# Performance work log

Measured on AMD Instinct MI355X. Metric: run time of the kernel, lower is better.

Reference implementation:

```python
import jax, jax.numpy as jnp
import numpy as np

B, N, K, C = 8, 4096, 32, 64
RADIUS = 0.15
CIN = C + 3  # dp_fj: concat(dp[3], fj[C])


def _ball_query(p, radius, k):
    """p: (B,N,3). Returns neighbor indices (B,N,K): first k points (in index
    order) within radius of each query, padded with the first valid neighbor
    (ballquery semantics; query point itself is always index 0 candidate)."""
    sq = jnp.sum(p * p, axis=-1)                                  # (B,N)
    d2 = sq[:, :, None] + sq[:, None, :] - 2.0 * jnp.einsum('bnd,bmd->bnm', p, p)
    n = p.shape[1]
    within = d2 <= radius * radius
    key = jnp.where(within, jnp.arange(n, dtype=jnp.int32)[None, None, :], n)
    order = jnp.argsort(key, axis=-1)[..., :k]                    # (B,N,K)
    valid = jnp.take_along_axis(key, order, axis=-1) < n
    first = order[..., :1]
    return jnp.where(valid, order, first)


def _conv2d_1x1(x, w, b):
    # x: (B,Cin,N,K), w: (Cout,Cin), b: (Cout,)
    return jnp.einsum('oi,bink->bonk', w, x) + b[None, :, None, None]


def _conv1d_1x1(x, w, b):
    # x: (B,Cin,N)
    return jnp.einsum('oi,bin->bon', w, x) + b[None, :, None]


def setup_inputs() -> dict:
    key = jax.random.key(0)
    ks = jax.random.split(key, 16)
    s = 0.05
    inp = {
        'p': jax.random.uniform(ks[0], (B, N, 3), dtype=jnp.float32),
        'f': jax.random.normal(ks[1], (B, C, N), dtype=jnp.float32),
        # attn_local: convblock2d (CIN -> C), no act
        'w_attn': jax.random.normal(ks[2], (C, CIN), dtype=jnp.float32) * s,
        'b_attn': jnp.zeros((C,), jnp.float32),
        # convs: convblock2d (CIN -> C, relu) then (C -> C, no act)
        'w1': jax.random.normal(ks[3], (C, CIN), dtype=jnp.float32) * s,
        'b1': jnp.zeros((C,), jnp.float32),
        'w2': jax.random.normal(ks[4], (C, C), dtype=jnp.float32) * s,
        'b2': jnp.zeros((C,), jnp.float32),
        # ffn: convblock1d (C -> C*expansion=C, relu) then (C -> C, no act)
        'wf1': jax.random.normal(ks[5], (C, C), dtype=jnp.float32) * s,
        'bf1': jnp.zeros((C,), jnp.float32),
        'wf2': jax.random.normal(ks[6], (C, C), dtype=jnp.float32) * s,
        'bf2': jnp.zeros((C,), jnp.float32),
    }
    return inp


def reference(p, f, w_attn, b_attn, w1, b1, w2, b2, wf1, bf1, wf2, bf2):
    bidx = jnp.arange(B)[:, None, None]
    idx = _ball_query(p, RADIUS, K)                               # (B,N,K) int
    pj = p[bidx, idx]                                             # (B,N,K,3)
    dp = (pj - p[:, :, None, :]).transpose(0, 3, 1, 2)            # (B,3,N,K)
    ft = f.transpose(0, 2, 1)                                     # (B,N,C)
    fj = ft[bidx, idx].transpose(0, 3, 1, 2)                      # (B,C,N,K)

    fj_cat = jnp.concatenate([dp, fj], axis=1)                    # (B,CIN,N,K)

    attn = _conv2d_1x1(fj_cat, w_attn, b_attn)                    # (B,C,N,K)
    x = jax.nn.relu(_conv2d_1x1(fj_cat, w1, b1))
    x = _conv2d_1x1(x, w2, b2)                                    # (B,C,N,K)

    # new_attention, 4D path: softmax over neighbor axis (tau=1), weighted sum
    channel_attn = jax.nn.softmax(attn, axis=-1)
    fout = jnp.sum(channel_attn * x, axis=-1)                     # (B,C,N)

    fout = jax.nn.relu(fout + f)
    identity = fout
    h = jax.nn.relu(_conv1d_1x1(fout, wf1, bf1))
    h = _conv1d_1x1(h, wf2, bf2)
    fout = jax.nn.relu(h + identity)                              # use_res
    return (p, fout)
```

## Files before the change

### kernel.cpp

```cpp
#include <hip/hip_runtime.h>

#define B_ 8
#define N_ 4096
#define K_ 32
#define C_ 64
#define CIN_ 67
#define R2_ 0.0225f

#define SFJ 104
#define SY1 72
#define SFB 72
#define PTS 4
#define ITERS 4

typedef short short8v __attribute__((ext_vector_type(8)));
typedef short short4v __attribute__((ext_vector_type(4)));
typedef float floatx4 __attribute__((ext_vector_type(4)));

__device__ __forceinline__ short f2bf(float x) {
    unsigned u = __float_as_uint(x);
    u += 0x7fffu + ((u >> 16) & 1u);
    return (short)(u >> 16);
}

template <int CTRL>
__device__ __forceinline__ float dpp_add(float x) {
    const int m = __builtin_amdgcn_update_dpp(0, __float_as_int(x), CTRL, 0xF, 0xF, false);
    return x + __int_as_float(m);
}
__device__ __forceinline__ float row16_sum(float x) {
    x = dpp_add<0xB1>(x);
    x = dpp_add<0x4E>(x);
    x = dpp_add<0x141>(x);
    x = dpp_add<0x140>(x);
    return x;
}

__global__ __launch_bounds__(256) void prep_kernel(
    const float* __restrict__ p, const float* __restrict__ f,
    unsigned short* __restrict__ ftb, float4* __restrict__ p4,
    float* __restrict__ pout)
{
#pragma clang fp contract(off)
    __shared__ short tile[64 * 72];
    const int t = threadIdx.x;
    const int b = blockIdx.x >> 6;
    const int n0 = (blockIdx.x & 63) * 64;
    const int nn4 = t & 15, ch = t >> 4;
    for (int cc = 0; cc < 4; ++cc) {
        const int c = cc * 16 + ch;
        const float4 v = *(const float4*)&f[((size_t)(b * 64 + c)) * N_ + n0 + nn4 * 4];
        tile[(nn4 * 4 + 0) * 72 + c] = f2bf(v.x);
        tile[(nn4 * 4 + 1) * 72 + c] = f2bf(v.y);
        tile[(nn4 * 4 + 2) * 72 + c] = f2bf(v.z);
        tile[(nn4 * 4 + 3) * 72 + c] = f2bf(v.w);
    }
    if (t < 48) {
        const size_t base = ((size_t)(b * N_ + n0)) * 3;
        ((float4*)(pout + base))[t] = ((const float4*)(p + base))[t];
    }
    if (t < 64) {
        const int n = n0 + t;
        const float x = p[((size_t)(b * N_ + n)) * 3 + 0];
        const float y = p[((size_t)(b * N_ + n)) * 3 + 1];
        const float z = p[((size_t)(b * N_ + n)) * 3 + 2];
        const float sq = (x * x + y * y) + z * z;
        p4[(size_t)b * N_ + n] = make_float4(x, y, z, sq);
    }
    __syncthreads();
    const int nn = t >> 2, cb = (t & 3) * 16;
    uint4* dst = (uint4*)&ftb[((size_t)(b * N_ + n0 + nn)) * 64 + cb];
    const uint4* src = (const uint4*)&tile[nn * 72 + cb];
    dst[0] = src[0];
    dst[1] = src[1];
}

__global__ __launch_bounds__(256) void ball_query_kernel(
    const float4* __restrict__ p4, unsigned short* __restrict__ idx)
{
#pragma clang fp contract(off)
    const int lane = threadIdx.x & 63;
    const int wid = (blockIdx.x * blockDim.x + threadIdx.x) >> 6;
    const int q0 = wid * 4;
    const int b = q0 >> 12;
    const float4* pb = p4 + (size_t)b * N_;

    float4 Q[4];
    #pragma unroll
    for (int q = 0; q < 4; ++q)
        Q[q] = pb[(q0 + q) & (N_ - 1)];
    int count[4] = {0, 0, 0, 0};
    int first[4] = {-1, -1, -1, -1};
    for (int base = 0; base < N_; base += 64) {
        const float4 A = pb[base + lane];
        unsigned long long m[4];
        bool w[4];
        #pragma unroll
        for (int q = 0; q < 4; ++q) {
            const float d2 = (Q[q].w + A.w)
                - 2.0f * ((Q[q].x * A.x + Q[q].y * A.y) + Q[q].z * A.z);
            w[q] = (d2 <= R2_);
            m[q] = __ballot(w[q]);
        }
        const unsigned long long below = (1ull << lane) - 1ull;
        #pragma unroll
        for (int q = 0; q < 4; ++q) {
            if (m[q]) {
                if (first[q] < 0) first[q] = base + __builtin_ctzll(m[q]);
                if (w[q]) {
                    const int pos = count[q] + __popcll(m[q] & below);
                    if (pos < K_)
                        idx[(size_t)(q0 + q) * K_ + pos] = (unsigned short)(base + lane);
                }
                count[q] += __popcll(m[q]);
            }
        }
        if (count[0] >= K_ && count[1] >= K_ && count[2] >= K_ && count[3] >= K_)
            break;
    }
    #pragma unroll
    for (int q = 0; q < 4; ++q)
        for (int pos = count[q] + lane; pos < K_; pos += 64)
            idx[(size_t)(q0 + q) * K_ + pos] = (unsigned short)first[q];
}

__global__ __launch_bounds__(256, 3) void lpa_mfma_kernel(
    const float4* __restrict__ p4, const float* __restrict__ f,
    const unsigned short* __restrict__ ftb,
    const float* __restrict__ w_attn, const float* __restrict__ b_attn,
    const float* __restrict__ w1, const float* __restrict__ b1,
    const float* __restrict__ w2, const float* __restrict__ b2,
    const float* __restrict__ wf1, const float* __restrict__ bf1,
    const float* __restrict__ wf2, const float* __restrict__ bf2,
    const unsigned short* __restrict__ idx, float* __restrict__ out)
{
    __shared__ __align__(16) short s_fj[128 * SFJ];
    __shared__ __align__(16) short s_y1[128 * SY1];
    __shared__ __align__(16) short s_fbuf[2 * 16 * SFB];
    __shared__ float s_vec[PTS * 64];
    short* s_vecbf = s_fbuf;
    short* s_hbf   = s_fbuf + 16 * SFB;

    const int t = threadIdx.x;
    const int lane = t & 63;
    const int mb = t >> 6;
    const int l15 = lane & 15;
    const int quad = lane >> 4;

    short8v wa_f[3], w1_f[3], w2_f[2], wf1_f[2], wf2_f[2];
    {
        const int cm = mb * 16 + l15;
        #pragma unroll
        for (int ks = 0; ks < 3; ++ks) {
            short8v a, bq;
            #pragma unroll
            for (int j = 0; j < 8; ++j) {
                const int ip = ks * 32 + quad * 8 + j;
                float va = 0.0f, vb = 0.0f;
                if (ip < 64)      { va = w_attn[cm * CIN_ + ip + 3];  vb = w1[cm * CIN_ + ip + 3]; }
                else if (ip < 67) { va = w_attn[cm * CIN_ + ip - 64]; vb = w1[cm * CIN_ + ip - 64]; }
                a[j] = f2bf(va); bq[j] = f2bf(vb);
            }
            wa_f[ks] = a; w1_f[ks] = bq;
        }
        #pragma unroll
        for (int ks = 0; ks < 2; ++ks) {
            short8v a, bq, cq;
            #pragma unroll
            for (int j = 0; j < 8; ++j) {
                const int kk = ks * 32 + quad * 8 + j;
                a[j]  = f2bf(w2[cm * 64 + kk]);
                bq[j] = f2bf(wf1[cm * 64 + kk]);
                cq[j] = f2bf(wf2[cm * 64 + kk]);
            }
            w2_f[ks] = a; wf1_f[ks] = bq; wf2_f[ks] = cq;
        }
    }

    const int crow = mb * 16 + quad * 4;
    const float4 bav  = *(const float4*)&b_attn[crow];
    const float4 b1v  = *(const float4*)&b1[crow];
    const float4 b2v  = *(const float4*)&b2[crow];
    const float4 bf1v = *(const float4*)&bf1[crow];
    const float4 bf2v = *(const float4*)&bf2[crow];

    for (int e = t; e < 512; e += 256) {
        const int col = e >> 2, c4 = e & 3;
        *(uint4*)&s_fj[col * SFJ + 72 + c4 * 8] = make_uint4(0u, 0u, 0u, 0u);
    }
    for (int e = t; e < 1152; e += 256) ((unsigned*)s_fbuf)[e] = 0u;

    const int pt00 = blockIdx.x * (PTS * ITERS);
    const int bb = pt00 >> 12;
    const float4* pb = p4 + (size_t)bb * N_;

    for (int itn = 0; itn < ITERS; ++itn) {
        const int pt0 = pt00 + itn * PTS;

        {
            const int col = t >> 1, h = t & 1;
            const int j = idx[(size_t)pt0 * K_ + col];
            const uint4* src = (const uint4*)&ftb[((size_t)(bb * N_ + j)) * 64 + h * 32];
            uint4* dst = (uint4*)&s_fj[col * SFJ + h * 32];
            dst[0] = src[0]; dst[1] = src[1]; dst[2] = src[2]; dst[3] = src[3];
            if (h) {
                const int n = (pt0 + (col >> 5)) & (N_ - 1);
                const float4 Pj = pb[j];
                const float4 Pn = pb[n];
                short8v dp = {};
                dp[0] = f2bf(Pj.x - Pn.x);
                dp[1] = f2bf(Pj.y - Pn.y);
                dp[2] = f2bf(Pj.z - Pn.z);
                *(short8v*)&s_fj[col * SFJ + 64] = dp;
            }
        }
        __syncthreads();

        floatx4 accA[8];
        #pragma unroll
        for (int nt = 0; nt < 8; ++nt) {
            const short* bp = &s_fj[(nt * 16 + l15) * SFJ + quad * 8];
            const short8v fb0 = *(const short8v*)(bp);
            const short8v fb1 = *(const short8v*)(bp + 32);
            const short8v fb2 = *(const short8v*)(bp + 64);
            floatx4 a = {0.f, 0.f, 0.f, 0.f};
            a = __builtin_amdgcn_mfma_f32_16x16x32_bf16(wa_f[0], fb0, a, 0, 0, 0);
            a = __builtin_amdgcn_mfma_f32_16x16x32_bf16(wa_f[1], fb1, a, 0, 0, 0);
            a = __builtin_amdgcn_mfma_f32_16x16x32_bf16(wa_f[2], fb2, a, 0, 0, 0);
            accA[nt] = a;
            floatx4 y = {0.f, 0.f, 0.f, 0.f};
            y = __builtin_amdgcn_mfma_f32_16x16x32_bf16(w1_f[0], fb0, y, 0, 0, 0);
            y = __builtin_amdgcn_mfma_f32_16x16x32_bf16(w1_f[1], fb1, y, 0, 0, 0);
            y = __builtin_amdgcn_mfma_f32_16x16x32_bf16(w1_f[2], fb2, y, 0, 0, 0);
            short4v yp;
            yp[0] = f2bf(fmaxf(y[0] + b1v.x, 0.f));
            yp[1] = f2bf(fmaxf(y[1] + b1v.y, 0.f));
            yp[2] = f2bf(fmaxf(y[2] + b1v.z, 0.f));
            yp[3] = f2bf(fmaxf(y[3] + b1v.w, 0.f));
            *(short4v*)&s_y1[(nt * 16 + l15) * SY1 + crow] = yp;
        }
        __syncthreads();

        floatx4 accX[8];
        #pragma unroll
        for (int nt = 0; nt < 8; ++nt) {
            const short* bp = &s_y1[(nt * 16 + l15) * SY1 + quad * 8];
            const short8v yb0 = *(const short8v*)(bp);
            const short8v yb1 = *(const short8v*)(bp + 32);
            floatx4 x = {0.f, 0.f, 0.f, 0.f};
            x = __builtin_amdgcn_mfma_f32_16x16x32_bf16(w2_f[0], yb0, x, 0, 0, 0);
            x = __builtin_amdgcn_mfma_f32_16x16x32_bf16(w2_f[1], yb1, x, 0, 0, 0);
            accX[nt] = x;
        }

        #pragma unroll
        for (int pi = 0; pi < PTS; ++pi) {
            const int n = (pt0 + pi) & (N_ - 1);
            float fo[4];
            #pragma unroll
            for (int r = 0; r < 4; ++r) {
                const float ba = (r == 0) ? bav.x : (r == 1) ? bav.y : (r == 2) ? bav.z : bav.w;
                const float bx = (r == 0) ? b2v.x : (r == 1) ? b2v.y : (r == 2) ? b2v.z : b2v.w;
                const float e0 = __expf(accA[2 * pi][r] + ba);
                const float e1 = __expf(accA[2 * pi + 1][r] + ba);
                const float se = row16_sum(e0 + e1);
                const float sw = row16_sum(e0 * (accX[2 * pi][r] + bx)
                                         + e1 * (accX[2 * pi + 1][r] + bx));
                const float fres = f[((size_t)(bb * 64 + crow + r)) * N_ + n];
                fo[r] = fmaxf(sw * __builtin_amdgcn_rcpf(se) + fres, 0.f);
            }
            if (l15 == 0) {
                *(float4*)&s_vec[pi * 64 + crow] = make_float4(fo[0], fo[1], fo[2], fo[3]);
                short4v fb;
                fb[0] = f2bf(fo[0]); fb[1] = f2bf(fo[1]);
                fb[2] = f2bf(fo[2]); fb[3] = f2bf(fo[3]);
                *(short4v*)&s_vecbf[pi * SFB + crow] = fb;
            }
        }
        __syncthreads();

        {
            const short8v vb0 = *(const short8v*)&s_vecbf[l15 * SFB + quad * 8];
            const short8v vb1 = *(const short8v*)&s_vecbf[l15 * SFB + 32 + quad * 8];
            floatx4 d = {0.f, 0.f, 0.f, 0.f};
            d = __builtin_amdgcn_mfma_f32_16x16x32_bf16(wf1_f[0], vb0, d, 0, 0, 0);
            d = __builtin_amdgcn_mfma_f32_16x16x32_bf16(wf1_f[1], vb1, d, 0, 0, 0);
            if (l15 < PTS) {
                short4v hb;
                hb[0] = f2bf(fmaxf(d[0] + bf1v.x, 0.f));
                hb[1] = f2bf(fmaxf(d[1] + bf1v.y, 0.f));
                hb[2] = f2bf(fmaxf(d[2] + bf1v.z, 0.f));
                hb[3] = f2bf(fmaxf(d[3] + bf1v.w, 0.f));
                *(short4v*)&s_hbf[l15 * SFB + crow] = hb;
            }
        }
        __syncthreads();

        {
            const short8v hb0 = *(const short8v*)&s_hbf[l15 * SFB + quad * 8];
            const short8v hb1 = *(const short8v*)&s_hbf[l15 * SFB + 32 + quad * 8];
            floatx4 d = {0.f, 0.f, 0.f, 0.f};
            d = __builtin_amdgcn_mfma_f32_16x16x32_bf16(wf2_f[0], hb0, d, 0, 0, 0);
            d = __builtin_amdgcn_mfma_f32_16x16x32_bf16(wf2_f[1], hb1, d, 0, 0, 0);
            if (l15 < PTS) {
                const int n = (pt0 + l15) & (N_ - 1);
                out[((size_t)(bb * 64 + crow + 0)) * N_ + n] =
                    fmaxf(d[0] + bf2v.x + s_vec[l15 * 64 + crow + 0], 0.f);
                out[((size_t)(bb * 64 + crow + 1)) * N_ + n] =
                    fmaxf(d[1] + bf2v.y + s_vec[l15 * 64 + crow + 1], 0.f);
                out[((size_t)(bb * 64 + crow + 2)) * N_ + n] =
                    fmaxf(d[2] + bf2v.z + s_vec[l15 * 64 + crow + 2], 0.f);
                out[((size_t)(bb * 64 + crow + 3)) * N_ + n] =
                    fmaxf(d[3] + bf2v.w + s_vec[l15 * 64 + crow + 3], 0.f);
            }
        }
    }
}

extern "C" void kernel_launch(void* const* d_in, const int* in_sizes, int n_in,
                              void* d_out, int out_size, void* d_ws, size_t ws_size,
                              hipStream_t stream)
{
    const float* p      = (const float*)d_in[0];
    const float* f      = (const float*)d_in[1];
    const float* w_attn = (const float*)d_in[2];
    const float* b_attn = (const float*)d_in[3];
    const float* w1     = (const float*)d_in[4];
    const float* b1     = (const float*)d_in[5];
    const float* w2     = (const float*)d_in[6];
    const float* b2     = (const float*)d_in[7];
    const float* wf1    = (const float*)d_in[8];
    const float* bf1    = (const float*)d_in[9];
    const float* wf2    = (const float*)d_in[10];
    const float* bf2    = (const float*)d_in[11];
    float* out = (float*)d_out;

    unsigned short* idx = (unsigned short*)d_ws;
    unsigned short* ftb = (unsigned short*)((char*)d_ws + 2u * 1024 * 1024);
    float4* p4          = (float4*)((char*)d_ws + 6u * 1024 * 1024);

    prep_kernel<<<B_ * (N_ / 64), 256, 0, stream>>>(p, f, ftb, p4, out);
    ball_query_kernel<<<(B_ * N_) / 16, 256, 0, stream>>>(p4, idx);
    lpa_mfma_kernel<<<(B_ * N_) / (PTS * ITERS), 256, 0, stream>>>(
        p4, f, ftb, w_attn, b_attn, w1, b1, w2, b2, wf1, bf1, wf2, bf2,
        idx, out + (size_t)B_ * N_ * 3);
}
```

Baseline: 229.6 us.

## Replace padded LDS tiles with XOR-swizzled layout and split dp buffer

Drops the padded row strides in shared memory and uses unpadded 64-element rows with an XOR swizzle on 8-element chunks, so MFMA operand loads and stores avoid bank conflicts with less LDS. The three dp channels move to a separate small buffer that only quad 0 feeds into the third K-slice, which removes the zero-padding of the feature tile. Launch bounds rise from 3 to 4 blocks per SM to use the freed LDS for occupancy, at the risk of more register pressure.

```diff
diff --git a/kernel.cpp b/kernel.cpp
--- a/kernel.cpp
+++ b/kernel.cpp
@@ -7,9 +7,6 @@
 #define CIN_ 67
 #define R2_ 0.0225f
 
-#define SFJ 104
-#define SY1 72
-#define SFB 72
 #define PTS 4
 #define ITERS 4
 
@@ -124,7 +121,7 @@
             idx[(size_t)(q0 + q) * K_ + pos] = (unsigned short)first[q];
 }
 
-__global__ __launch_bounds__(256, 3) void lpa_mfma_kernel(
+__global__ __launch_bounds__(256, 4) void lpa_mfma_kernel(
     const float4* __restrict__ p4, const float* __restrict__ f,
     const unsigned short* __restrict__ ftb,
     const float* __restrict__ w_attn, const float* __restrict__ b_attn,
@@ -134,12 +131,13 @@
     const float* __restrict__ wf2, const float* __restrict__ bf2,
     const unsigned short* __restrict__ idx, float* __restrict__ out)
 {
-    __shared__ __align__(16) short s_fj[128 * SFJ];
-    __shared__ __align__(16) short s_y1[128 * SY1];
-    __shared__ __align__(16) short s_fbuf[2 * 16 * SFB];
+    __shared__ __align__(16) short s_fj[128 * 64];
+    __shared__ __align__(16) short s_dp[128 * 8];
+    __shared__ __align__(16) short s_y1[128 * 64];
+    __shared__ __align__(16) short s_fbuf[2 * 16 * 64];
     __shared__ float s_vec[PTS * 64];
     short* s_vecbf = s_fbuf;
-    short* s_hbf   = s_fbuf + 16 * SFB;
+    short* s_hbf   = s_fbuf + 16 * 64;
 
     const int t = threadIdx.x;
     const int lane = t & 63;
@@ -184,11 +182,7 @@
     const float4 bf1v = *(const float4*)&bf1[crow];
     const float4 bf2v = *(const float4*)&bf2[crow];
 
-    for (int e = t; e < 512; e += 256) {
-        const int col = e >> 2, c4 = e & 3;
-        *(uint4*)&s_fj[col * SFJ + 72 + c4 * 8] = make_uint4(0u, 0u, 0u, 0u);
-    }
-    for (int e = t; e < 1152; e += 256) ((unsigned*)s_fbuf)[e] = 0u;
+    for (int e = t; e < 1024; e += 256) ((unsigned*)s_fbuf)[e] = 0u;
 
     const int pt00 = blockIdx.x * (PTS * ITERS);
     const int bb = pt00 >> 12;
@@ -201,8 +195,12 @@
             const int col = t >> 1, h = t & 1;
             const int j = idx[(size_t)pt0 * K_ + col];
             const uint4* src = (const uint4*)&ftb[((size_t)(bb * N_ + j)) * 64 + h * 32];
-            uint4* dst = (uint4*)&s_fj[col * SFJ + h * 32];
-            dst[0] = src[0]; dst[1] = src[1]; dst[2] = src[2]; dst[3] = src[3];
+            const int rb = col * 64;
+            const int sw = (col & 7) << 3;
+            *(uint4*)&s_fj[rb + ((h * 32 + 0)  ^ sw)] = src[0];
+            *(uint4*)&s_fj[rb + ((h * 32 + 8)  ^ sw)] = src[1];
+            *(uint4*)&s_fj[rb + ((h * 32 + 16) ^ sw)] = src[2];
+            *(uint4*)&s_fj[rb + ((h * 32 + 24) ^ sw)] = src[3];
             if (h) {
                 const int n = (pt0 + (col >> 5)) & (N_ - 1);
                 const float4 Pj = pb[j];
@@ -211,7 +209,7 @@
                 dp[0] = f2bf(Pj.x - Pn.x);
                 dp[1] = f2bf(Pj.y - Pn.y);
                 dp[2] = f2bf(Pj.z - Pn.z);
-                *(short8v*)&s_fj[col * SFJ + 64] = dp;
+                *(short8v*)&s_dp[col * 8] = dp;
             }
         }
         __syncthreads();
@@ -219,10 +217,14 @@
         floatx4 accA[8];
         #pragma unroll
         for (int nt = 0; nt < 8; ++nt) {
-            const short* bp = &s_fj[(nt * 16 + l15) * SFJ + quad * 8];
-            const short8v fb0 = *(const short8v*)(bp);
-            const short8v fb1 = *(const short8v*)(bp + 32);
-            const short8v fb2 = *(const short8v*)(bp + 64);
+            const int row = nt * 16 + l15;
+            const int sw = (l15 & 7) << 3;
+            const short* bp = &s_fj[row * 64];
+            const short8v fb0 = *(const short8v*)(bp + ((quad * 8) ^ sw));
+            const short8v fb1 = *(const short8v*)(bp + ((32 + quad * 8) ^ sw));
+            const short8v dpv = *(const short8v*)&s_dp[row * 8];
+            short8v fb2 = {};
+            if (quad == 0) fb2 = dpv;
             floatx4 a = {0.f, 0.f, 0.f, 0.f};
             a = __builtin_amdgcn_mfma_f32_16x16x32_bf16(wa_f[0], fb0, a, 0, 0, 0);
             a = __builtin_amdgcn_mfma_f32_16x16x32_bf16(wa_f[1], fb1, a, 0, 0, 0);
@@ -237,16 +239,18 @@
             yp[1] = f2bf(fmaxf(y[1] + b1v.y, 0.f));
             yp[2] = f2bf(fmaxf(y[2] + b1v.z, 0.f));
             yp[3] = f2bf(fmaxf(y[3] + b1v.w, 0.f));
-            *(short4v*)&s_y1[(nt * 16 + l15) * SY1 + crow] = yp;
+            *(short4v*)&s_y1[row * 64 + (crow ^ sw)] = yp;
         }
         __syncthreads();
 
         floatx4 accX[8];
         #pragma unroll
         for (int nt = 0; nt < 8; ++nt) {
-            const short* bp = &s_y1[(nt * 16 + l15) * SY1 + quad * 8];
-            const short8v yb0 = *(const short8v*)(bp);
-            const short8v yb1 = *(const short8v*)(bp + 32);
+            const int row = nt * 16 + l15;
+            const int sw = (l15 & 7) << 3;
+            const short* bp = &s_y1[row * 64];
+            const short8v yb0 = *(const short8v*)(bp + ((quad * 8) ^ sw));
+            const short8v yb1 = *(const short8v*)(bp + ((32 + quad * 8) ^ sw));
             floatx4 x = {0.f, 0.f, 0.f, 0.f};
             x = __builtin_amdgcn_mfma_f32_16x16x32_bf16(w2_f[0], yb0, x, 0, 0, 0);
             x = __builtin_amdgcn_mfma_f32_16x16x32_bf16(w2_f[1], yb1, x, 0, 0, 0);
@@ -264,24 +268,25 @@
                 const float e0 = __expf(accA[2 * pi][r] + ba);
                 const float e1 = __expf(accA[2 * pi + 1][r] + ba);
                 const float se = row16_sum(e0 + e1);
-                const float sw = row16_sum(e0 * (accX[2 * pi][r] + bx)
-                                         + e1 * (accX[2 * pi + 1][r] + bx));
+                const float sw_ = row16_sum(e0 * (accX[2 * pi][r] + bx)
+                                          + e1 * (accX[2 * pi + 1][r] + bx));
                 const float fres = f[((size_t)(bb * 64 + crow + r)) * N_ + n];
-                fo[r] = fmaxf(sw * __builtin_amdgcn_rcpf(se) + fres, 0.f);
+                fo[r] = fmaxf(sw_ * __builtin_amdgcn_rcpf(se) + fres, 0.f);
             }
             if (l15 == 0) {
                 *(float4*)&s_vec[pi * 64 + crow] = make_float4(fo[0], fo[1], fo[2], fo[3]);
                 short4v fb;
                 fb[0] = f2bf(fo[0]); fb[1] = f2bf(fo[1]);
                 fb[2] = f2bf(fo[2]); fb[3] = f2bf(fo[3]);
-                *(short4v*)&s_vecbf[pi * SFB + crow] = fb;
+                *(short4v*)&s_vecbf[pi * 64 + (crow ^ ((pi & 7) << 3))] = fb;
             }
         }
         __syncthreads();
 
         {
-            const short8v vb0 = *(const short8v*)&s_vecbf[l15 * SFB + quad * 8];
-            const short8v vb1 = *(const short8v*)&s_vecbf[l15 * SFB + 32 + quad * 8];
+            const int sw = (l15 & 7) << 3;
+            const short8v vb0 = *(const short8v*)&s_vecbf[l15 * 64 + ((quad * 8) ^ sw)];
+            const short8v vb1 = *(const short8v*)&s_vecbf[l15 * 64 + ((32 + quad * 8) ^ sw)];
             floatx4 d = {0.f, 0.f, 0.f, 0.f};
             d = __builtin_amdgcn_mfma_f32_16x16x32_bf16(wf1_f[0], vb0, d, 0, 0, 0);
             d = __builtin_amdgcn_mfma_f32_16x16x32_bf16(wf1_f[1], vb1, d, 0, 0, 0);
@@ -291,14 +296,15 @@
                 hb[1] = f2bf(fmaxf(d[1] + bf1v.y, 0.f));
                 hb[2] = f2bf(fmaxf(d[2] + bf1v.z, 0.f));
                 hb[3] = f2bf(fmaxf(d[3] + bf1v.w, 0.f));
-                *(short4v*)&s_hbf[l15 * SFB + crow] = hb;
+                *(short4v*)&s_hbf[l15 * 64 + (crow ^ sw)] = hb;
             }
         }
         __syncthreads();
 
         {
-            const short8v hb0 = *(const short8v*)&s_hbf[l15 * SFB + quad * 8];
-            const short8v hb1 = *(const short8v*)&s_hbf[l15 * SFB + 32 + quad * 8];
+            const int sw = (l15 & 7) << 3;
+            const short8v hb0 = *(const short8v*)&s_hbf[l15 * 64 + ((quad * 8) ^ sw)];
+            const short8v hb1 = *(const short8v*)&s_hbf[l15 * 64 + ((32 + quad * 8) ^ sw)];
             floatx4 d = {0.f, 0.f, 0.f, 0.f};
             d = __builtin_amdgcn_mfma_f32_16x16x32_bf16(wf2_f[0], hb0, d, 0, 0, 0);
             d = __builtin_amdgcn_mfma_f32_16x16x32_bf16(wf2_f[1], hb1, d, 0, 0, 0);
```

New measurement: 387.0 us. +68.5%, slower.

## Prefetch next iteration's neighbor gather into registers and interleave second conv with softmax

Applied to the files above, without the earlier changes.

Hoists the first neighbor-feature gather out of the loop and, inside each iteration, issues global loads for the next iteration's gathered features and positions into registers before the MFMA work, writing them to shared memory after the first conv. This hides gather latency and removes one barrier per iteration. The second conv is now computed per point inside the softmax loop, which cuts live accumulator registers. The residual f values are loaded as float4 vectors. It also drops the occupancy hint of 3 blocks in the launch bounds, so prefetch registers may raise register pressure and lower occupancy.

```diff
diff --git a/kernel.cpp b/kernel.cpp
--- a/kernel.cpp
+++ b/kernel.cpp
@@ -124,7 +124,7 @@
             idx[(size_t)(q0 + q) * K_ + pos] = (unsigned short)first[q];
 }
 
-__global__ __launch_bounds__(256, 3) void lpa_mfma_kernel(
+__global__ __launch_bounds__(256) void lpa_mfma_kernel(
     const float4* __restrict__ p4, const float* __restrict__ f,
     const unsigned short* __restrict__ ftb,
     const float* __restrict__ w_attn, const float* __restrict__ b_attn,
@@ -194,27 +194,39 @@
     const int bb = pt00 >> 12;
     const float4* pb = p4 + (size_t)bb * N_;
 
+    const int col = t >> 1, h = t & 1;
+
+    {
+        const int j = idx[(size_t)pt00 * K_ + col];
+        const uint4* src = (const uint4*)&ftb[((size_t)(bb * N_ + j)) * 64 + h * 32];
+        uint4* dst = (uint4*)&s_fj[col * SFJ + h * 32];
+        dst[0] = src[0]; dst[1] = src[1]; dst[2] = src[2]; dst[3] = src[3];
+        if (h) {
+            const int n = (pt00 + (col >> 5)) & (N_ - 1);
+            const float4 Pj = pb[j];
+            const float4 Pn = pb[n];
+            short8v dp = {};
+            dp[0] = f2bf(Pj.x - Pn.x);
+            dp[1] = f2bf(Pj.y - Pn.y);
+            dp[2] = f2bf(Pj.z - Pn.z);
+            *(short8v*)&s_fj[col * SFJ + 64] = dp;
+        }
+    }
+    __syncthreads();
+
     for (int itn = 0; itn < ITERS; ++itn) {
         const int pt0 = pt00 + itn * PTS;
 
-        {
-            const int col = t >> 1, h = t & 1;
-            const int j = idx[(size_t)pt0 * K_ + col];
-            const uint4* src = (const uint4*)&ftb[((size_t)(bb * N_ + j)) * 64 + h * 32];
-            uint4* dst = (uint4*)&s_fj[col * SFJ + h * 32];
-            dst[0] = src[0]; dst[1] = src[1]; dst[2] = src[2]; dst[3] = src[3];
-            if (h) {
-                const int n = (pt0 + (col >> 5)) & (N_ - 1);
-                const float4 Pj = pb[j];
-                const float4 Pn = pb[n];
-                short8v dp = {};
-                dp[0] = f2bf(Pj.x - Pn.x);
-                dp[1] = f2bf(Pj.y - Pn.y);
-                dp[2] = f2bf(Pj.z - Pn.z);
-                *(short8v*)&s_fj[col * SFJ + 64] = dp;
-            }
-        }
-        __syncthreads();
+        const bool pf = (itn + 1 < ITERS);
+        uint4 g0, g1, g2, g3;
+        float4 Pjn, Pnn;
+        if (pf) {
+            const int jn = idx[(size_t)(pt0 + PTS) * K_ + col];
+            const uint4* src = (const uint4*)&ftb[((size_t)(bb * N_ + jn)) * 64 + h * 32];
+            g0 = src[0]; g1 = src[1]; g2 = src[2]; g3 = src[3];
+            Pjn = pb[jn];
+            Pnn = pb[(pt0 + PTS + (col >> 5)) & (N_ - 1)];
+        }
 
         floatx4 accA[8];
         #pragma unroll
@@ -241,21 +253,45 @@
         }
         __syncthreads();
 
-        floatx4 accX[8];
-        #pragma unroll
-        for (int nt = 0; nt < 8; ++nt) {
-            const short* bp = &s_y1[(nt * 16 + l15) * SY1 + quad * 8];
-            const short8v yb0 = *(const short8v*)(bp);
-            const short8v yb1 = *(const short8v*)(bp + 32);
-            floatx4 x = {0.f, 0.f, 0.f, 0.f};
-            x = __builtin_amdgcn_mfma_f32_16x16x32_bf16(w2_f[0], yb0, x, 0, 0, 0);
-            x = __builtin_amdgcn_mfma_f32_16x16x32_bf16(w2_f[1], yb1, x, 0, 0, 0);
-            accX[nt] = x;
-        }
+        if (pf) {
+            uint4* dst = (uint4*)&s_fj[col * SFJ + h * 32];
+            dst[0] = g0; dst[1] = g1; dst[2] = g2; dst[3] = g3;
+            if (h) {
+                short8v dp = {};
+                dp[0] = f2bf(Pjn.x - Pnn.x);
+                dp[1] = f2bf(Pjn.y - Pnn.y);
+                dp[2] = f2bf(Pjn.z - Pnn.z);
+                *(short8v*)&s_fj[col * SFJ + 64] = dp;
+            }
+        }
+
+        const int nb0 = pt0 & (N_ - 1);
+        float4 f4r[4];
+        #pragma unroll
+        for (int r = 0; r < 4; ++r)
+            f4r[r] = *(const float4*)&f[((size_t)(bb * 64 + crow + r)) * N_ + nb0];
 
         #pragma unroll
         for (int pi = 0; pi < PTS; ++pi) {
-            const int n = (pt0 + pi) & (N_ - 1);
+            floatx4 xx0, xx1;
+            {
+                const short* bp = &s_y1[((2 * pi) * 16 + l15) * SY1 + quad * 8];
+                const short8v yb0 = *(const short8v*)(bp);
+                const short8v yb1 = *(const short8v*)(bp + 32);
+                floatx4 x = {0.f, 0.f, 0.f, 0.f};
+                x = __builtin_amdgcn_mfma_f32_16x16x32_bf16(w2_f[0], yb0, x, 0, 0, 0);
+                x = __builtin_amdgcn_mfma_f32_16x16x32_bf16(w2_f[1], yb1, x, 0, 0, 0);
+                xx0 = x;
+            }
+            {
+                const short* bp = &s_y1[((2 * pi + 1) * 16 + l15) * SY1 + quad * 8];
+                const short8v yb0 = *(const short8v*)(bp);
+                const short8v yb1 = *(const short8v*)(bp + 32);
+                floatx4 x = {0.f, 0.f, 0.f, 0.f};
+                x = __builtin_amdgcn_mfma_f32_16x16x32_bf16(w2_f[0], yb0, x, 0, 0, 0);
+                x = __builtin_amdgcn_mfma_f32_16x16x32_bf16(w2_f[1], yb1, x, 0, 0, 0);
+                xx1 = x;
+            }
             float fo[4];
             #pragma unroll
             for (int r = 0; r < 4; ++r) {
@@ -264,9 +300,9 @@
                 const float e0 = __expf(accA[2 * pi][r] + ba);
                 const float e1 = __expf(accA[2 * pi + 1][r] + ba);
                 const float se = row16_sum(e0 + e1);
-                const float sw = row16_sum(e0 * (accX[2 * pi][r] + bx)
-                                         + e1 * (accX[2 * pi + 1][r] + bx));
-                const float fres = f[((size_t)(bb * 64 + crow + r)) * N_ + n];
+                const float sw = row16_sum(e0 * (xx0[r] + bx) + e1 * (xx1[r] + bx));
+                const float fres = (pi == 0) ? f4r[r].x : (pi == 1) ? f4r[r].y
+                                 : (pi == 2) ? f4r[r].z : f4r[r].w;
                 fo[r] = fmaxf(sw * __builtin_amdgcn_rcpf(se) + fres, 0.f);
             }
             if (l15 == 0) {
```

After: 226.3 us. No clear change (-1.5%).
